# Optimization experiments

Hardware: AMD Instinct MI355X
Metric: run time of the kernel (lower is better)

## Reference

```python
import jax, jax.numpy as jnp
import numpy as np


def setup_inputs() -> dict:
    key = jax.random.key(0)
    k1, k2, k3 = jax.random.split(key, 3)
    B, H, W = 4, 1024, 1024
    D, Hg, Wg = 8, 16, 16
    C = 12  # (Cin+1)*Cout = (3+1)*3
    grid = jax.random.normal(k1, (B, C, D, Hg, Wg), dtype=jnp.float32)
    guide = jax.random.uniform(k2, (B, H, W), dtype=jnp.float32)
    image = jax.random.normal(k3, (B, 3, H, W), dtype=jnp.float32)
    return {"grid": grid, "guide": guide, "image": image}


def _slice_coeffs(grid, guide):
    """Guide-indexed trilinear slice of the bilateral grid.

    grid:  [B, C, D, Hg, Wg]; guide: [B, H, W] in [0,1].
    Returns per-pixel coefficients [B, H, W, C].
    """
    B, C, D, Hg, Wg = grid.shape
    _, H, W = guide.shape
    grid_t = jnp.transpose(grid, (0, 2, 3, 4, 1))  # [B, D, Hg, Wg, C]

    # grid-space coordinates of each pixel (HDRNet convention)
    gx = (jnp.arange(W, dtype=grid.dtype) + 0.5) * Wg / W   # [W]
    gy = (jnp.arange(H, dtype=grid.dtype) + 0.5) * Hg / H   # [H]
    gz = guide * D                                          # [B, H, W]

    fx = jnp.floor(gx - 0.5)
    fy = jnp.floor(gy - 0.5)
    fz = jnp.floor(gz - 0.5)

    bb = jnp.arange(B)[:, None, None]
    coeff = jnp.zeros((B, H, W, C), dtype=grid.dtype)
    for dz in (0, 1):
        zz = fz + dz
        wz = jnp.maximum(1.0 - jnp.abs(zz + 0.5 - gz), 0.0)     # [B,H,W]
        zi = jnp.clip(zz, 0, D - 1).astype(jnp.int32)
        for dy in (0, 1):
            yy = fy + dy
            wy = jnp.maximum(1.0 - jnp.abs(yy + 0.5 - gy), 0.0)  # [H]
            yi = jnp.clip(yy, 0, Hg - 1).astype(jnp.int32)
            for dx in (0, 1):
                xx = fx + dx
                wx = jnp.maximum(1.0 - jnp.abs(xx + 0.5 - gx), 0.0)  # [W]
                xi = jnp.clip(xx, 0, Wg - 1).astype(jnp.int32)
                w = wz * wy[None, :, None] * wx[None, None, :]       # [B,H,W]
                c = grid_t[bb, zi, yi[None, :, None], xi[None, None, :]]  # [B,H,W,C]
                coeff = coeff + w[..., None] * c
    return coeff


def reference(grid, guide, image):
    B, Cin, H, W = image.shape
    coeff = _slice_coeffs(grid, guide)                 # [B,H,W,(Cin+1)*Cout]
    Cout = coeff.shape[-1] // (Cin + 1)
    coeff = coeff.reshape(B, H, W, Cout, Cin + 1)
    # per-pixel affine: out[c] = sum_j A[c,j] * image[j] + bias[c]
    out = jnp.einsum('bhwcj,bjhw->bchw', coeff[..., :Cin], image)
    out = out + jnp.transpose(coeff[..., Cin], (0, 3, 1, 2))
    return out
```

## Files before the change

kernel.cpp:

```cpp
#include <hip/hip_runtime.h>

#define BB 4
#define CC 12
#define DD 8
#define HG 16
#define WG 16
#define HH 1024
#define WW 1024

typedef float vf4 __attribute__((ext_vector_type(4)));
typedef _Float16 h4 __attribute__((ext_vector_type(4)));
typedef _Float16 h2 __attribute__((ext_vector_type(2)));

#define XSTRH 104
#define ROWS 2
#define NSTG 3

__global__ __launch_bounds__(256, 4) void slice_apply(
    const float* __restrict__ grid,
    const float* __restrict__ guide,
    const float* __restrict__ img,
    float* __restrict__ out)
{
    __shared__ _Float16 S[ROWS * WG * XSTRH];

    const int blk = blockIdx.x;
    const int b  = blk >> 9;
    const int h0 = (blk & 511) * ROWS;

    const float gy0 = (h0 + 0.5f) * ((float)HG / (float)HH);
    const float fy  = floorf(gy0 - 0.5f);
    const int   iy0 = max(0, min(HG - 1, (int)fy));
    const int   iy1 = max(0, min(HG - 1, (int)fy + 1));

    float wy1r[ROWS];
    #pragma unroll
    for (int r = 0; r < ROWS; ++r) {
        const float gy = (h0 + r + 0.5f) * ((float)HG / (float)HH);
        wy1r[r] = gy - 0.5f - fy;
    }

    float a0[NSTG], a1[NSTG], c0v[NSTG], c1v[NSTG];
    int   so[NSTG];
    #pragma unroll
    for (int t = 0; t < NSTG; ++t) {
        const int j = (int)threadIdx.x + t * 256;
        const int x = j & 15;
        const int z = (j >> 4) & 7;
        const int pr = j >> 7;
        const size_t base0 = ((size_t)(b * CC + 2 * pr) * DD + z) * (HG * WG);
        const size_t base1 = ((size_t)(b * CC + 2 * pr + 1) * DD + z) * (HG * WG);
        a0[t] = grid[base0 + iy0 * WG + x];
        a1[t] = grid[base0 + iy1 * WG + x];
        c0v[t] = grid[base1 + iy0 * WG + x];
        c1v[t] = grid[base1 + iy1 * WG + x];
        so[t] = x * XSTRH + z * 12 + 2 * pr;
    }

    const int w0 = (int)threadIdx.x * 4;
    vf4 g4[ROWS], i0[ROWS], i1[ROWS], i2[ROWS];
    #pragma unroll
    for (int r = 0; r < ROWS; ++r) {
        const size_t pix = ((size_t)b * HH + (h0 + r)) * WW + w0;
        g4[r] = *reinterpret_cast<const vf4*>(guide + pix);
        const float* ib = img + (((size_t)b * 3) * HH + (h0 + r)) * WW + w0;
        i0[r] = __builtin_nontemporal_load(reinterpret_cast<const vf4*>(ib));
        i1[r] = __builtin_nontemporal_load(reinterpret_cast<const vf4*>(ib + (size_t)HH * WW));
        i2[r] = __builtin_nontemporal_load(reinterpret_cast<const vf4*>(ib + (size_t)2 * HH * WW));
    }

    #pragma unroll
    for (int t = 0; t < NSTG; ++t) {
        const float d0 = a1[t] - a0[t];
        const float d1 = c1v[t] - c0v[t];
        #pragma unroll
        for (int r = 0; r < ROWS; ++r) {
            const float f0 = a0[t] + wy1r[r] * d0;
            const float f1 = c0v[t] + wy1r[r] * d1;
            h2 v; v[0] = (_Float16)f0; v[1] = (_Float16)f1;
            *reinterpret_cast<h2*>(&S[r * (WG * XSTRH) + so[t]]) = v;
        }
    }
    __syncthreads();

    const float scale = (float)WG / (float)WW;
    const float gx0 = (w0 + 0.5f) * scale;
    const float fx  = floorf(gx0 - 0.5f);
    const float tx0 = gx0 - 0.5f - fx;
    const int   ix0 = max(0, min(WG - 1, (int)fx));
    const int   ix1 = max(0, min(WG - 1, (int)fx + 1));

    #pragma unroll
    for (int r = 0; r < ROWS; ++r) {
        const int h = h0 + r;
        const _Float16* Sr  = S + r * (WG * XSTRH);
        const _Float16* Sx0 = Sr + ix0 * XSTRH;
        const _Float16* Sx1 = Sr + ix1 * XSTRH;

        vf4 o0, o1, o2;

        #pragma unroll
        for (int p = 0; p < 4; ++p) {
            const float tx  = tx0 + (float)p * scale;
            const float wx0 = 1.0f - tx, wx1 = tx;

            const float gv = g4[r][p];
            const float gz  = gv * (float)DD;
            const float fz  = floorf(gz - 0.5f);
            const float tz  = gz - 0.5f - fz;
            const int   iz0 = max(0, min(DD - 1, (int)fz));
            const int   iz1 = max(0, min(DD - 1, (int)fz + 1));
            const float wz0 = 1.0f - tz, wz1 = tz;

            const float w00 = wz0 * wx0, w01 = wz0 * wx1;
            const float w10 = wz1 * wx0, w11 = wz1 * wx1;

            float acc[12];
            #pragma unroll
            for (int k = 0; k < 12; ++k) acc[k] = 0.0f;

            auto accum = [&](const _Float16* P, float w) {
                const h4 a = *reinterpret_cast<const h4*>(P);
                const h4 e = *reinterpret_cast<const h4*>(P + 4);
                const h4 f = *reinterpret_cast<const h4*>(P + 8);
                #pragma unroll
                for (int k = 0; k < 4; ++k) {
                    acc[k]     += w * (float)a[k];
                    acc[4 + k] += w * (float)e[k];
                    acc[8 + k] += w * (float)f[k];
                }
            };
            accum(Sx0 + iz0 * 12, w00);
            accum(Sx1 + iz0 * 12, w01);
            accum(Sx0 + iz1 * 12, w10);
            accum(Sx1 + iz1 * 12, w11);

            const float im0 = i0[r][p];
            const float im1 = i1[r][p];
            const float im2 = i2[r][p];

            o0[p] = acc[0] * im0 + acc[1] * im1 + acc[2]  * im2 + acc[3];
            o1[p] = acc[4] * im0 + acc[5] * im1 + acc[6]  * im2 + acc[7];
            o2[p] = acc[8] * im0 + acc[9] * im1 + acc[10] * im2 + acc[11];
        }

        float* ob = out + (((size_t)b * 3) * HH + h) * WW + w0;
        *reinterpret_cast<vf4*>(ob) = o0;
        *reinterpret_cast<vf4*>(ob + (size_t)HH * WW) = o1;
        *reinterpret_cast<vf4*>(ob + (size_t)2 * HH * WW) = o2;
    }
}

extern "C" void kernel_launch(void* const* d_in, const int* in_sizes, int n_in,
                              void* d_out, int out_size, void* d_ws, size_t ws_size,
                              hipStream_t stream) {
    const float* grid  = (const float*)d_in[0];
    const float* guide = (const float*)d_in[1];
    const float* image = (const float*)d_in[2];
    float* out = (float*)d_out;

    const int nblocks = BB * HH / ROWS;
    slice_apply<<<nblocks, 256, 0, stream>>>(grid, guide, image, out);
}
```

Baseline: 117.7 us.

## Process one row per block and raise occupancy launch bound

Each block now handles one image row instead of two. This halves shared memory and the per-thread image/guide registers, and the launch bound rises from 4 to 6 waves-per-EU hint to allow more resident blocks and hide memory latency. In exchange, each block does the grid row-slice staging (12 scattered grid loads per thread plus a barrier) for only one row, doubling that fixed overhead, and the block count doubles.

```diff
diff --git a/kernel.cpp b/kernel.cpp
--- a/kernel.cpp
+++ b/kernel.cpp
@@ -13,32 +13,25 @@
 typedef _Float16 h2 __attribute__((ext_vector_type(2)));
 
 #define XSTRH 104
-#define ROWS 2
 #define NSTG 3
 
-__global__ __launch_bounds__(256, 4) void slice_apply(
+__global__ __launch_bounds__(256, 6) void slice_apply(
     const float* __restrict__ grid,
     const float* __restrict__ guide,
     const float* __restrict__ img,
     float* __restrict__ out)
 {
-    __shared__ _Float16 S[ROWS * WG * XSTRH];
+    __shared__ _Float16 S[WG * XSTRH];
 
     const int blk = blockIdx.x;
-    const int b  = blk >> 9;
-    const int h0 = (blk & 511) * ROWS;
+    const int b = blk >> 10;
+    const int h = blk & 1023;
 
-    const float gy0 = (h0 + 0.5f) * ((float)HG / (float)HH);
-    const float fy  = floorf(gy0 - 0.5f);
+    const float gy = (h + 0.5f) * ((float)HG / (float)HH);
+    const float fy = floorf(gy - 0.5f);
+    const float ty = gy - 0.5f - fy;
     const int   iy0 = max(0, min(HG - 1, (int)fy));
     const int   iy1 = max(0, min(HG - 1, (int)fy + 1));
-
-    float wy1r[ROWS];
-    #pragma unroll
-    for (int r = 0; r < ROWS; ++r) {
-        const float gy = (h0 + r + 0.5f) * ((float)HG / (float)HH);
-        wy1r[r] = gy - 0.5f - fy;
-    }
 
     float a0[NSTG], a1[NSTG], c0v[NSTG], c1v[NSTG];
     int   so[NSTG];
@@ -58,28 +51,19 @@
     }
 
     const int w0 = (int)threadIdx.x * 4;
-    vf4 g4[ROWS], i0[ROWS], i1[ROWS], i2[ROWS];
-    #pragma unroll
-    for (int r = 0; r < ROWS; ++r) {
-        const size_t pix = ((size_t)b * HH + (h0 + r)) * WW + w0;
-        g4[r] = *reinterpret_cast<const vf4*>(guide + pix);
-        const float* ib = img + (((size_t)b * 3) * HH + (h0 + r)) * WW + w0;
-        i0[r] = __builtin_nontemporal_load(reinterpret_cast<const vf4*>(ib));
-        i1[r] = __builtin_nontemporal_load(reinterpret_cast<const vf4*>(ib + (size_t)HH * WW));
-        i2[r] = __builtin_nontemporal_load(reinterpret_cast<const vf4*>(ib + (size_t)2 * HH * WW));
-    }
+    const size_t pix = ((size_t)b * HH + h) * WW + w0;
+    const vf4 g4 = *reinterpret_cast<const vf4*>(guide + pix);
+    const float* ib = img + (((size_t)b * 3) * HH + h) * WW + w0;
+    const vf4 i0 = __builtin_nontemporal_load(reinterpret_cast<const vf4*>(ib));
+    const vf4 i1 = __builtin_nontemporal_load(reinterpret_cast<const vf4*>(ib + (size_t)HH * WW));
+    const vf4 i2 = __builtin_nontemporal_load(reinterpret_cast<const vf4*>(ib + (size_t)2 * HH * WW));
 
     #pragma unroll
     for (int t = 0; t < NSTG; ++t) {
-        const float d0 = a1[t] - a0[t];
-        const float d1 = c1v[t] - c0v[t];
-        #pragma unroll
-        for (int r = 0; r < ROWS; ++r) {
-            const float f0 = a0[t] + wy1r[r] * d0;
-            const float f1 = c0v[t] + wy1r[r] * d1;
-            h2 v; v[0] = (_Float16)f0; v[1] = (_Float16)f1;
-            *reinterpret_cast<h2*>(&S[r * (WG * XSTRH) + so[t]]) = v;
-        }
+        const float f0 = a0[t] + ty * (a1[t] - a0[t]);
+        const float f1 = c0v[t] + ty * (c1v[t] - c0v[t]);
+        h2 v; v[0] = (_Float16)f0; v[1] = (_Float16)f1;
+        *reinterpret_cast<h2*>(&S[so[t]]) = v;
     }
     __syncthreads();
 
@@ -89,66 +73,57 @@
     const float tx0 = gx0 - 0.5f - fx;
     const int   ix0 = max(0, min(WG - 1, (int)fx));
     const int   ix1 = max(0, min(WG - 1, (int)fx + 1));
+    const _Float16* Sx0 = S + ix0 * XSTRH;
+    const _Float16* Sx1 = S + ix1 * XSTRH;
+
+    vf4 o0, o1, o2;
 
     #pragma unroll
-    for (int r = 0; r < ROWS; ++r) {
-        const int h = h0 + r;
-        const _Float16* Sr  = S + r * (WG * XSTRH);
-        const _Float16* Sx0 = Sr + ix0 * XSTRH;
-        const _Float16* Sx1 = Sr + ix1 * XSTRH;
+    for (int p = 0; p < 4; ++p) {
+        const float tx  = tx0 + (float)p * scale;
+        const float wx0 = 1.0f - tx, wx1 = tx;
 
-        vf4 o0, o1, o2;
+        const float gz  = g4[p] * (float)DD;
+        const float fz  = floorf(gz - 0.5f);
+        const float tz  = gz - 0.5f - fz;
+        const int   ifz = (int)fz;
+        const int   iz0 = max(0, min(DD - 1, ifz));
+        const int   iz1 = max(0, min(DD - 1, ifz + 1));
+        const float wz0 = 1.0f - tz, wz1 = tz;
 
+        const float w00 = wz0 * wx0, w01 = wz0 * wx1;
+        const float w10 = wz1 * wx0, w11 = wz1 * wx1;
+
+        float acc[12];
         #pragma unroll
-        for (int p = 0; p < 4; ++p) {
-            const float tx  = tx0 + (float)p * scale;
-            const float wx0 = 1.0f - tx, wx1 = tx;
+        for (int k = 0; k < 12; ++k) acc[k] = 0.0f;
 
-            const float gv = g4[r][p];
-            const float gz  = gv * (float)DD;
-            const float fz  = floorf(gz - 0.5f);
-            const float tz  = gz - 0.5f - fz;
-            const int   iz0 = max(0, min(DD - 1, (int)fz));
-            const int   iz1 = max(0, min(DD - 1, (int)fz + 1));
-            const float wz0 = 1.0f - tz, wz1 = tz;
+        auto accum = [&](const _Float16* P, float w) {
+            const h4 a = *reinterpret_cast<const h4*>(P);
+            const h4 e = *reinterpret_cast<const h4*>(P + 4);
+            const h4 f = *reinterpret_cast<const h4*>(P + 8);
+            #pragma unroll
+            for (int k = 0; k < 4; ++k) {
+                acc[k]     += w * (float)a[k];
+                acc[4 + k] += w * (float)e[k];
+                acc[8 + k] += w * (float)f[k];
+            }
+        };
+        accum(Sx0 + iz0 * 12, w00);
+        accum(Sx1 + iz0 * 12, w01);
+        accum(Sx0 + iz1 * 12, w10);
+        accum(Sx1 + iz1 * 12, w11);
 
-            const float w00 = wz0 * wx0, w01 = wz0 * wx1;
-            const float w10 = wz1 * wx0, w11 = wz1 * wx1;
+        const float im0 = i0[p], im1 = i1[p], im2 = i2[p];
+        o0[p] = acc[0] * im0 + acc[1] * im1 + acc[2]  * im2 + acc[3];
+        o1[p] = acc[4] * im0 + acc[5] * im1 + acc[6]  * im2 + acc[7];
+        o2[p] = acc[8] * im0 + acc[9] * im1 + acc[10] * im2 + acc[11];
+    }
 
-            float acc[12];
-            #pragma unroll
-            for (int k = 0; k < 12; ++k) acc[k] = 0.0f;
-
-            auto accum = [&](const _Float16* P, float w) {
-                const h4 a = *reinterpret_cast<const h4*>(P);
-                const h4 e = *reinterpret_cast<const h4*>(P + 4);
-                const h4 f = *reinterpret_cast<const h4*>(P + 8);
-                #pragma unroll
-                for (int k = 0; k < 4; ++k) {
-                    acc[k]     += w * (float)a[k];
-                    acc[4 + k] += w * (float)e[k];
-                    acc[8 + k] += w * (float)f[k];
-                }
-            };
-            accum(Sx0 + iz0 * 12, w00);
-            accum(Sx1 + iz0 * 12, w01);
-            accum(Sx0 + iz1 * 12, w10);
-            accum(Sx1 + iz1 * 12, w11);
-
-            const float im0 = i0[r][p];
-            const float im1 = i1[r][p];
-            const float im2 = i2[r][p];
-
-            o0[p] = acc[0] * im0 + acc[1] * im1 + acc[2]  * im2 + acc[3];
-            o1[p] = acc[4] * im0 + acc[5] * im1 + acc[6]  * im2 + acc[7];
-            o2[p] = acc[8] * im0 + acc[9] * im1 + acc[10] * im2 + acc[11];
-        }
-
-        float* ob = out + (((size_t)b * 3) * HH + h) * WW + w0;
-        *reinterpret_cast<vf4*>(ob) = o0;
-        *reinterpret_cast<vf4*>(ob + (size_t)HH * WW) = o1;
-        *reinterpret_cast<vf4*>(ob + (size_t)2 * HH * WW) = o2;
-    }
+    float* ob = out + (((size_t)b * 3) * HH + h) * WW + w0;
+    *reinterpret_cast<vf4*>(ob) = o0;
+    *reinterpret_cast<vf4*>(ob + (size_t)HH * WW) = o1;
+    *reinterpret_cast<vf4*>(ob + (size_t)2 * HH * WW) = o2;
 }
 
 extern "C" void kernel_launch(void* const* d_in, const int* in_sizes, int n_in,
@@ -159,6 +134,6 @@
     const float* image = (const float*)d_in[2];
     float* out = (float*)d_out;
 
-    const int nblocks = BB * HH / ROWS;
+    const int nblocks = BB * HH;
     slice_apply<<<nblocks, 256, 0, stream>>>(grid, guide, image, out);
 }
```

Result: no change. 119.0 us (+1.1%).

## Process four rows per block with software-pipelined loads of second row pair

Applied to the files above, without the earlier changes.

Each block now covers four image rows instead of two, so the grid-slice loads are spread over more rows and half as many blocks are launched. The guide and image loads for rows 2-3 are issued before rows 0-1 are computed, overlapping that memory latency with compute. This raises register pressure from the extra live vectors and doubles shared memory per block, which may lower occupancy under the launch bounds.

```diff
diff --git a/kernel.cpp b/kernel.cpp
--- a/kernel.cpp
+++ b/kernel.cpp
@@ -13,7 +13,7 @@
 typedef _Float16 h2 __attribute__((ext_vector_type(2)));
 
 #define XSTRH 104
-#define ROWS 2
+#define ROWSB 4
 #define NSTG 3
 
 __global__ __launch_bounds__(256, 4) void slice_apply(
@@ -22,22 +22,22 @@
     const float* __restrict__ img,
     float* __restrict__ out)
 {
-    __shared__ _Float16 S[ROWS * WG * XSTRH];
+    __shared__ _Float16 S[ROWSB * WG * XSTRH];
 
     const int blk = blockIdx.x;
-    const int b  = blk >> 9;
-    const int h0 = (blk & 511) * ROWS;
+    const int b  = blk >> 8;
+    const int h0 = (blk & 255) * ROWSB;
 
     const float gy0 = (h0 + 0.5f) * ((float)HG / (float)HH);
     const float fy  = floorf(gy0 - 0.5f);
     const int   iy0 = max(0, min(HG - 1, (int)fy));
     const int   iy1 = max(0, min(HG - 1, (int)fy + 1));
 
-    float wy1r[ROWS];
+    float tyr[ROWSB];
     #pragma unroll
-    for (int r = 0; r < ROWS; ++r) {
+    for (int r = 0; r < ROWSB; ++r) {
         const float gy = (h0 + r + 0.5f) * ((float)HG / (float)HH);
-        wy1r[r] = gy - 0.5f - fy;
+        tyr[r] = gy - 0.5f - fy;
     }
 
     float a0[NSTG], a1[NSTG], c0v[NSTG], c1v[NSTG];
@@ -58,29 +58,37 @@
     }
 
     const int w0 = (int)threadIdx.x * 4;
-    vf4 g4[ROWS], i0[ROWS], i1[ROWS], i2[ROWS];
-    #pragma unroll
-    for (int r = 0; r < ROWS; ++r) {
+
+    auto loadrow = [&](int r, vf4& G, vf4& I0, vf4& I1, vf4& I2) {
         const size_t pix = ((size_t)b * HH + (h0 + r)) * WW + w0;
-        g4[r] = *reinterpret_cast<const vf4*>(guide + pix);
+        G = *reinterpret_cast<const vf4*>(guide + pix);
         const float* ib = img + (((size_t)b * 3) * HH + (h0 + r)) * WW + w0;
-        i0[r] = __builtin_nontemporal_load(reinterpret_cast<const vf4*>(ib));
-        i1[r] = __builtin_nontemporal_load(reinterpret_cast<const vf4*>(ib + (size_t)HH * WW));
-        i2[r] = __builtin_nontemporal_load(reinterpret_cast<const vf4*>(ib + (size_t)2 * HH * WW));
-    }
+        I0 = __builtin_nontemporal_load(reinterpret_cast<const vf4*>(ib));
+        I1 = __builtin_nontemporal_load(reinterpret_cast<const vf4*>(ib + (size_t)HH * WW));
+        I2 = __builtin_nontemporal_load(reinterpret_cast<const vf4*>(ib + (size_t)2 * HH * WW));
+    };
 
-    #pragma unroll
-    for (int t = 0; t < NSTG; ++t) {
-        const float d0 = a1[t] - a0[t];
-        const float d1 = c1v[t] - c0v[t];
+    auto fold2 = [&](int r0) {
         #pragma unroll
-        for (int r = 0; r < ROWS; ++r) {
-            const float f0 = a0[t] + wy1r[r] * d0;
-            const float f1 = c0v[t] + wy1r[r] * d1;
-            h2 v; v[0] = (_Float16)f0; v[1] = (_Float16)f1;
-            *reinterpret_cast<h2*>(&S[r * (WG * XSTRH) + so[t]]) = v;
+        for (int t = 0; t < NSTG; ++t) {
+            const float d0 = a1[t] - a0[t];
+            const float d1 = c1v[t] - c0v[t];
+            #pragma unroll
+            for (int rr = 0; rr < 2; ++rr) {
+                const float ty = tyr[r0 + rr];
+                h2 v;
+                v[0] = (_Float16)(a0[t] + ty * d0);
+                v[1] = (_Float16)(c0v[t] + ty * d1);
+                *reinterpret_cast<h2*>(&S[(r0 + rr) * (WG * XSTRH) + so[t]]) = v;
+            }
         }
-    }
+    };
+
+    vf4 gA0, iA00, iA01, iA02, gA1, iA10, iA11, iA12;
+    loadrow(0, gA0, iA00, iA01, iA02);
+    loadrow(1, gA1, iA10, iA11, iA12);
+
+    fold2(0);
     __syncthreads();
 
     const float scale = (float)WG / (float)WW;
@@ -90,26 +98,23 @@
     const int   ix0 = max(0, min(WG - 1, (int)fx));
     const int   ix1 = max(0, min(WG - 1, (int)fx + 1));
 
-    #pragma unroll
-    for (int r = 0; r < ROWS; ++r) {
-        const int h = h0 + r;
+    auto computerow = [&](int r, const vf4& G, const vf4& I0, const vf4& I1, const vf4& I2) {
         const _Float16* Sr  = S + r * (WG * XSTRH);
         const _Float16* Sx0 = Sr + ix0 * XSTRH;
         const _Float16* Sx1 = Sr + ix1 * XSTRH;
 
         vf4 o0, o1, o2;
-
         #pragma unroll
         for (int p = 0; p < 4; ++p) {
             const float tx  = tx0 + (float)p * scale;
             const float wx0 = 1.0f - tx, wx1 = tx;
 
-            const float gv = g4[r][p];
-            const float gz  = gv * (float)DD;
+            const float gz  = G[p] * (float)DD;
             const float fz  = floorf(gz - 0.5f);
             const float tz  = gz - 0.5f - fz;
-            const int   iz0 = max(0, min(DD - 1, (int)fz));
-            const int   iz1 = max(0, min(DD - 1, (int)fz + 1));
+            const int   ifz = (int)fz;
+            const int   iz0 = max(0, min(DD - 1, ifz));
+            const int   iz1 = max(0, min(DD - 1, ifz + 1));
             const float wz0 = 1.0f - tz, wz1 = tz;
 
             const float w00 = wz0 * wx0, w01 = wz0 * wx1;
@@ -135,20 +140,30 @@
             accum(Sx0 + iz1 * 12, w10);
             accum(Sx1 + iz1 * 12, w11);
 
-            const float im0 = i0[r][p];
-            const float im1 = i1[r][p];
-            const float im2 = i2[r][p];
-
+            const float im0 = I0[p], im1 = I1[p], im2 = I2[p];
             o0[p] = acc[0] * im0 + acc[1] * im1 + acc[2]  * im2 + acc[3];
             o1[p] = acc[4] * im0 + acc[5] * im1 + acc[6]  * im2 + acc[7];
             o2[p] = acc[8] * im0 + acc[9] * im1 + acc[10] * im2 + acc[11];
         }
 
-        float* ob = out + (((size_t)b * 3) * HH + h) * WW + w0;
+        float* ob = out + (((size_t)b * 3) * HH + (h0 + r)) * WW + w0;
         *reinterpret_cast<vf4*>(ob) = o0;
         *reinterpret_cast<vf4*>(ob + (size_t)HH * WW) = o1;
         *reinterpret_cast<vf4*>(ob + (size_t)2 * HH * WW) = o2;
-    }
+    };
+
+    vf4 gB0, iB00, iB01, iB02, gB1, iB10, iB11, iB12;
+    loadrow(2, gB0, iB00, iB01, iB02);
+    loadrow(3, gB1, iB10, iB11, iB12);
+
+    computerow(0, gA0, iA00, iA01, iA02);
+    computerow(1, gA1, iA10, iA11, iA12);
+
+    fold2(2);
+    __syncthreads();
+
+    computerow(2, gB0, iB00, iB01, iB02);
+    computerow(3, gB1, iB10, iB11, iB12);
 }
 
 extern "C" void kernel_launch(void* const* d_in, const int* in_sizes, int n_in,
@@ -159,6 +174,6 @@
     const float* image = (const float*)d_in[2];
     float* out = (float*)d_out;
 
-    const int nblocks = BB * HH / ROWS;
+    const int nblocks = BB * HH / ROWSB;
     slice_apply<<<nblocks, 256, 0, stream>>>(grid, guide, image, out);
 }
```

New measurement: 118.6 us. About the same (+0.7%).
